# Kernel optimization log

Measured on AMD Instinct MI355X. Metric: run time of the kernel, lower is better.

Reference implementation:

```python
import jax, jax.numpy as jnp
import numpy as np

B, NPTS, NBOX = 16, 100000, 64
PTS_THRESHOLD = 2048          # topk voxels kept per scene
GT_THRESHOLD = 2.5            # distance multiplier
VOXEL_SIZE = 0.01
TENSOR_STRIDE = 8             # stride of the level being pruned
SIZE = TENSOR_STRIDE * VOXEL_SIZE  # 0.08, per-voxel cell size at this level


def setup_inputs() -> dict:
    key = jax.random.key(0)
    k1, k2, k3 = jax.random.split(key, 3)
    scores = jax.random.normal(k1, (B, NPTS), dtype=jnp.float32)
    points = jax.random.uniform(k2, (B, NPTS, 3), dtype=jnp.float32)
    gt_centers = jax.random.uniform(k3, (B, NBOX, 3), dtype=jnp.float32)
    return {"scores": scores, "points": points, "gt_centers": gt_centers}


def reference(scores, points, gt_centers):
    # --- per-batch topk score mask (MEFPN3D._get_score_mask) ---
    _, idx = jax.lax.top_k(scores, PTS_THRESHOLD)          # [B, K]
    score_mask = jnp.zeros(scores.shape, dtype=bool)
    score_mask = score_mask.at[jnp.arange(B)[:, None], idx].set(True)  # scatter True

    # --- gt distance mask (MEFPN3D._get_gt_mask) ---
    # distances: [B, Npts, n_boxes]
    diff = points[:, :, None, :] - gt_centers[:, None, :, :]
    distances = jnp.sqrt(jnp.sum(diff * diff, axis=-1))
    gt_mask = jnp.any(distances < SIZE * GT_THRESHOLD, axis=-1)        # [B, Npts]

    # --- combined prune mask (scatter of per-batch masks into global mask) ---
    prune_mask = jnp.logical_or(score_mask, gt_mask)

    # --- per-voxel sigmoid BCE loss, reduction='none' (CrossEntropyLoss use_sigmoid=True) ---
    target = gt_mask.astype(scores.dtype)
    losses = target * jax.nn.softplus(-scores) + (1.0 - target) * jax.nn.softplus(scores)
    return prune_mask, losses
```

## Files before the change

kernel.cpp:

```cpp
#include <hip/hip_runtime.h>
#include <hip/hip_bf16.h>
#include <stdint.h>

#define BB 16
#define NPTS 100000
#define NBOX 64
#define KTOP 2048
#define THRF 0.2f
#define C_LO 0.039984f
#define C_HI 0.040016f

#define SLICES 16
#define SLICE_SPAN 6272
#define SCAP 512
#define LIST_CAP 4096
#define CUT 0xC0000000u

#define CAND_OFF 0
#define CNT_OFF  (BB * SLICES * SCAP)
#define STATE_OFF (CNT_OFF + BB * SLICES)
#define TBOX_OFF  (STATE_OFF + BB * 2)

__device__ __forceinline__ uint32_t fmap(float f) {
    uint32_t b = __float_as_uint(f);
    return (b & 0x80000000u) ? ~b : (b | 0x80000000u);
}

__global__ __launch_bounds__(256) void cand_k(const float* __restrict__ scores,
                                              uint32_t* __restrict__ ws) {
    __shared__ uint32_t buf[SCAP];
    __shared__ uint32_t lcnt;
    const int b = blockIdx.y, sl = blockIdx.x, tid = threadIdx.x;
    if (tid == 0) lcnt = 0;
    __syncthreads();
    const int start = sl * SLICE_SPAN;
    const int nf4 = min(SLICE_SPAN, NPTS - start) >> 2;
    const float4* sc4 = reinterpret_cast<const float4*>(scores + (size_t)b * NPTS + start);
    for (int i4 = tid; i4 < nf4; i4 += 256) {
        const float4 v = sc4[i4];
        const uint32_t u[4] = {fmap(v.x), fmap(v.y), fmap(v.z), fmap(v.w)};
#pragma unroll
        for (int j = 0; j < 4; ++j) {
            if (u[j] >= CUT) {
                const uint32_t pos = atomicAdd(&lcnt, 1u);
                if (pos < SCAP) buf[pos] = u[j];
            }
        }
    }
    __syncthreads();
    const uint32_t c = lcnt;
    uint32_t* dst = ws + CAND_OFF + ((size_t)(b * SLICES + sl)) * SCAP;
    const uint32_t cw = c < SCAP ? c : SCAP;
    for (uint32_t i = tid; i < cw; i += 256) dst[i] = buf[i];
    if (tid == 0) ws[CNT_OFF + b * SLICES + sl] = c;
}

__device__ __forceinline__ void pick256(const uint32_t* __restrict__ hist,
                                        uint32_t* __restrict__ excl,
                                        int tid, int lane, uint32_t target,
                                        uint32_t* sBin, uint32_t* sKrem,
                                        uint32_t* sE, uint32_t* sTot, int wantE) {
    __syncthreads();
    if (tid < 64) {
        const uint32_t v0 = hist[4*tid], v1 = hist[4*tid+1], v2 = hist[4*tid+2], v3 = hist[4*tid+3];
        const uint32_t lt = v0 + v1 + v2 + v3;
        uint32_t x = lt;
#pragma unroll
        for (int off = 1; off < 64; off <<= 1) {
            const uint32_t y = __shfl_up(x, off);
            if (lane >= off) x += y;
        }
        const uint32_t ex = x - lt;
        excl[4*tid] = ex; excl[4*tid+1] = ex + v0;
        excl[4*tid+2] = ex + v0 + v1; excl[4*tid+3] = ex + v0 + v1 + v2;
        if (tid == 63) *sTot = x;
    }
    __syncthreads();
    {
        const uint32_t total = *sTot, lim = total - target;
        const uint32_t pe = excl[tid];
        const uint32_t pe1 = (tid == 255) ? total : excl[tid + 1];
        if (pe <= lim && pe1 > lim) {
            *sBin = (uint32_t)tid;
            *sKrem = target - (total - pe1);
            if (wantE) *sE = pe1 - pe;
        }
    }
    __syncthreads();
}

__global__ __launch_bounds__(256) void selfin_k(const float* __restrict__ scores,
                                                const float* __restrict__ ctrs,
                                                uint32_t* __restrict__ ws) {
    const int b = blockIdx.x, tid = threadIdx.x, w = tid >> 6, lane = tid & 63;
    __shared__ uint32_t list[LIST_CAP];
    __shared__ uint32_t h4[4][257];
    __shared__ uint32_t hist[256], excl[256];
    __shared__ uint32_t scnt[SLICES], soff[SLICES];
    __shared__ uint32_t wcnt[4];
    __shared__ uint32_t sBin, sKrem, sE, sTot, sIstar, sRun, sSpec, sUni, lcnt;

    const float* sc = scores + (size_t)b * NPTS;

    if (tid < NBOX) {
        const float cx = ctrs[(size_t)b * NBOX * 3 + 3 * tid];
        const float cy = ctrs[(size_t)b * NBOX * 3 + 3 * tid + 1];
        const float cz = ctrs[(size_t)b * NBOX * 3 + 3 * tid + 2];
        float4* TB = reinterpret_cast<float4*>(ws + TBOX_OFF) + b * NBOX;
        TB[tid] = make_float4(-2.0f * cx, -2.0f * cy, -2.0f * cz,
                              fmaf(cx, cx, fmaf(cy, cy, cz * cz)));
    }

    if (tid < SLICES) scnt[tid] = ws[CNT_OFF + b * SLICES + tid];
    __syncthreads();
    if (tid == 0) {
        uint32_t tot = 0; bool ok = true;
        for (int s = 0; s < SLICES; ++s) {
            soff[s] = tot;
            const uint32_t c = scnt[s];
            if (c > SCAP) ok = false;
            tot += c;
        }
        sTot = tot;
        sSpec = (ok && tot >= KTOP && tot <= LIST_CAP) ? 1u : 0u;
        sKrem = KTOP;
        sIstar = NPTS;
        lcnt = 0;
        sUni = 1u;
    }
    __syncthreads();

    uint32_t cnt, prefix = 0u;
    int shift0;
    if (sSpec) {
        cnt = sTot;
#pragma unroll 2
        for (int s = 0; s < SLICES; ++s) {
            const uint32_t c = scnt[s], o = soff[s];
            const uint32_t* src = ws + CAND_OFF + ((size_t)(b * SLICES + s)) * SCAP;
            for (uint32_t i = tid; i < c; i += 256) list[o + i] = src[i];
        }
        __syncthreads();
        const uint32_t b0 = list[0] >> 24;
        bool uni = true;
        for (uint32_t i = tid; i < cnt; i += 256) uni &= ((list[i] >> 24) == b0);
        if (!uni) atomicAnd(&sUni, 0u);
        __syncthreads();
        if (sUni) { prefix = b0 << 24; shift0 = 16; }
        else      { prefix = 0u;       shift0 = 24; }
    } else {
        for (int i = tid; i < 4 * 257; i += 256) (&h4[0][0])[i] = 0;
        __syncthreads();
        const float4* sc4 = reinterpret_cast<const float4*>(sc);
        for (int i4 = tid; i4 < NPTS / 4; i4 += 256) {
            const float4 v = sc4[i4];
            atomicAdd(&h4[w][fmap(v.x) >> 24], 1u);
            atomicAdd(&h4[w][fmap(v.y) >> 24], 1u);
            atomicAdd(&h4[w][fmap(v.z) >> 24], 1u);
            atomicAdd(&h4[w][fmap(v.w) >> 24], 1u);
        }
        __syncthreads();
        hist[tid] = h4[0][tid] + h4[1][tid] + h4[2][tid] + h4[3][tid];
        pick256(hist, excl, tid, lane, KTOP, &sBin, &sKrem, &sE, &sTot, 0);
        const uint32_t beta = sBin;
        for (int i4 = tid; i4 < NPTS / 4; i4 += 256) {
            const float4 v = sc4[i4];
            const uint32_t u[4] = {fmap(v.x), fmap(v.y), fmap(v.z), fmap(v.w)};
#pragma unroll
            for (int j = 0; j < 4; ++j) {
                if ((u[j] >> 24) == beta) {
                    const uint32_t pos = atomicAdd(&lcnt, 1u);
                    if (pos < LIST_CAP) list[pos] = u[j];
                }
            }
        }
        __syncthreads();
        cnt = lcnt < LIST_CAP ? lcnt : LIST_CAP;
        prefix = beta << 24;
        shift0 = 16;
    }

#pragma unroll 1
    for (int shift = shift0; shift >= 0; shift -= 8) {
        for (int i = tid; i < 4 * 257; i += 256) (&h4[0][0])[i] = 0;
        __syncthreads();
        const uint32_t hi8 = (shift < 24) ? (prefix >> (shift + 8)) : 0u;
        uint32_t* mh = h4[lane & 3];
        for (uint32_t i = tid; i < cnt; i += 256) {
            const uint32_t uu = list[i];
            const bool m = (shift == 24) || ((uu >> (shift + 8)) == hi8);
            if (m) atomicAdd(&mh[(uu >> shift) & 255u], 1u);
        }
        __syncthreads();
        hist[tid] = h4[0][tid] + h4[1][tid] + h4[2][tid] + h4[3][tid];
        const uint32_t target = sKrem;
        pick256(hist, excl, tid, lane, target, &sBin, &sKrem, &sE, &sTot,
                shift == 0 ? 1 : 0);
        prefix |= sBin << shift;
    }

    const uint32_t R = sKrem, E = sE;
    const uint32_t tbits = (prefix & 0x80000000u) ? (prefix & 0x7fffffffu) : ~prefix;

    if (E != R) {
        const float T = __uint_as_float(tbits);
        if (tid == 0) sRun = 0;
        __syncthreads();
        for (int base = 0; base < NPTS; base += 256) {
            const uint32_t r0 = sRun;
            if (r0 > R) break;
            const int i = base + tid;
            const bool eq = (i < NPTS) && (sc[i] == T);
            const unsigned long long mask = __ballot(eq);
            if (lane == 0) wcnt[w] = (uint32_t)__popcll(mask);
            __syncthreads();
            uint32_t before = 0, total = 0;
#pragma unroll
            for (int ww = 0; ww < 4; ++ww) {
                const uint32_t c = wcnt[ww];
                if (ww < w) before += c;
                total += c;
            }
            if (eq) {
                const uint32_t rank = r0 + before +
                    (uint32_t)__popcll(mask & ((1ull << lane) - 1ull));
                if (rank == R) sIstar = (uint32_t)i;
            }
            __syncthreads();
            if (tid == 0) sRun = r0 + total;
            __syncthreads();
        }
        __syncthreads();
    }
    if (tid == 0) {
        uint32_t* st = ws + STATE_OFF + b * 2;
        st[0] = tbits;
        st[1] = sIstar;
    }
}

__device__ __noinline__ bool exact_gt(float px, float py, float pz,
                                      const float* __restrict__ C) {
    bool hit = false;
#pragma unroll 1
    for (int k = 0; k < NBOX; ++k) {
        float dx = px - C[3 * k + 0];
        float dy = py - C[3 * k + 1];
        float dz = pz - C[3 * k + 2];
        float d2 = __fadd_rn(__fadd_rn(__fmul_rn(dx, dx), __fmul_rn(dy, dy)),
                             __fmul_rn(dz, dz));
        if (__fsqrt_rn(d2) < THRF) hit = true;
    }
    return hit;
}

__global__ __launch_bounds__(256) void main_k(const float* __restrict__ scores,
                                              const float* __restrict__ points,
                                              const float* __restrict__ ctrs,
                                              const uint32_t* __restrict__ ws,
                                              float* __restrict__ out) {
    const int b = blockIdx.y;
    const int i = blockIdx.x * 256 + threadIdx.x;
    if (i >= NPTS) return;

    const uint32_t* st = ws + STATE_OFF + b * 2;
    const float T = __uint_as_float(st[0]);
    const uint32_t Istar = st[1];
    const float4* __restrict__ TB =
        reinterpret_cast<const float4*>(ws + TBOX_OFF) + b * NBOX;

    const float* P = points + ((size_t)b * NPTS + i) * 3;
    const float px = P[0], py = P[1], pz = P[2];
    float m2 = 1e30f;

#pragma unroll
    for (int k = 0; k < NBOX; ++k) {
        const float4 B = TB[k];
        const float t = fmaf(B.x, px, fmaf(B.y, py, fmaf(B.z, pz, B.w)));
        m2 = fminf(m2, t);
    }

    const float s = scores[(size_t)b * NPTS + i];
    const float pp = fmaf(px, px, fmaf(py, py, pz * pz));
    const float m = pp + m2;
    bool gt;
    if (m < C_LO) gt = true;
    else if (m >= C_HI) gt = false;
    else gt = exact_gt(px, py, pz, ctrs + b * NBOX * 3);
    const bool sm = (s > T) || (s == T && (uint32_t)i < Istar);
    const float x = gt ? -s : s;
    const float ls = fmaxf(x, 0.0f) + __logf(1.0f + __expf(-fabsf(s)));
    out[(size_t)b * NPTS + i] = (gt || sm) ? 1.0f : 0.0f;
    out[(size_t)BB * NPTS + (size_t)b * NPTS + i] = ls;
}

extern "C" void kernel_launch(void* const* d_in, const int* in_sizes, int n_in,
                              void* d_out, int out_size, void* d_ws, size_t ws_size,
                              hipStream_t stream) {
    const float* scores = (const float*)d_in[0];
    const float* points = (const float*)d_in[1];
    const float* ctrs   = (const float*)d_in[2];
    float* out = (float*)d_out;
    uint32_t* ws = (uint32_t*)d_ws;

    const dim3 gridC(SLICES, BB);
    cand_k<<<gridC, 256, 0, stream>>>(scores, ws);
    selfin_k<<<BB, 256, 0, stream>>>(scores, ctrs, ws);
    const dim3 gridP((NPTS + 255) / 256, BB);
    main_k<<<gridP, 256, 0, stream>>>(scores, points, ctrs, ws, out);
}
```

Before: 47.70 us.

## Process eight points per thread in main kernel with vectorized loads and stores

The main kernel now has each thread handle eight consecutive points. It loads their coordinates and scores as float4 vectors and writes both outputs as float4 stores. Box centers are read directly from the input and shared across the eight points, so the precomputed box table in the selection kernel is dropped. This is meant to cut per-point load overhead, reuse box constants across points and widen memory transactions, at the cost of more registers and fewer threads.

```diff
diff --git a/kernel.cpp b/kernel.cpp
--- a/kernel.cpp
+++ b/kernel.cpp
@@ -19,7 +19,6 @@
 #define CAND_OFF 0
 #define CNT_OFF  (BB * SLICES * SCAP)
 #define STATE_OFF (CNT_OFF + BB * SLICES)
-#define TBOX_OFF  (STATE_OFF + BB * 2)
 
 __device__ __forceinline__ uint32_t fmap(float f) {
     uint32_t b = __float_as_uint(f);
@@ -99,18 +98,7 @@
     __shared__ uint32_t scnt[SLICES], soff[SLICES];
     __shared__ uint32_t wcnt[4];
     __shared__ uint32_t sBin, sKrem, sE, sTot, sIstar, sRun, sSpec, sUni, lcnt;
-
     const float* sc = scores + (size_t)b * NPTS;
-
-    if (tid < NBOX) {
-        const float cx = ctrs[(size_t)b * NBOX * 3 + 3 * tid];
-        const float cy = ctrs[(size_t)b * NBOX * 3 + 3 * tid + 1];
-        const float cz = ctrs[(size_t)b * NBOX * 3 + 3 * tid + 2];
-        float4* TB = reinterpret_cast<float4*>(ws + TBOX_OFF) + b * NBOX;
-        TB[tid] = make_float4(-2.0f * cx, -2.0f * cy, -2.0f * cz,
-                              fmaf(cx, cx, fmaf(cy, cy, cz * cz)));
-    }
-
     if (tid < SLICES) scnt[tid] = ws[CNT_OFF + b * SLICES + tid];
     __syncthreads();
     if (tid == 0) {
@@ -123,13 +111,9 @@
         }
         sTot = tot;
         sSpec = (ok && tot >= KTOP && tot <= LIST_CAP) ? 1u : 0u;
-        sKrem = KTOP;
-        sIstar = NPTS;
-        lcnt = 0;
-        sUni = 1u;
-    }
-    __syncthreads();
-
+        sKrem = KTOP; sIstar = NPTS; lcnt = 0; sUni = 1u;
+    }
+    __syncthreads();
     uint32_t cnt, prefix = 0u;
     int shift0;
     if (sSpec) {
@@ -176,10 +160,8 @@
         }
         __syncthreads();
         cnt = lcnt < LIST_CAP ? lcnt : LIST_CAP;
-        prefix = beta << 24;
-        shift0 = 16;
-    }
-
+        prefix = beta << 24; shift0 = 16;
+    }
 #pragma unroll 1
     for (int shift = shift0; shift >= 0; shift -= 8) {
         for (int i = tid; i < 4 * 257; i += 256) (&h4[0][0])[i] = 0;
@@ -194,14 +176,11 @@
         __syncthreads();
         hist[tid] = h4[0][tid] + h4[1][tid] + h4[2][tid] + h4[3][tid];
         const uint32_t target = sKrem;
-        pick256(hist, excl, tid, lane, target, &sBin, &sKrem, &sE, &sTot,
-                shift == 0 ? 1 : 0);
+        pick256(hist, excl, tid, lane, target, &sBin, &sKrem, &sE, &sTot, shift == 0 ? 1 : 0);
         prefix |= sBin << shift;
     }
-
     const uint32_t R = sKrem, E = sE;
     const uint32_t tbits = (prefix & 0x80000000u) ? (prefix & 0x7fffffffu) : ~prefix;
-
     if (E != R) {
         const float T = __uint_as_float(tbits);
         if (tid == 0) sRun = 0;
@@ -222,8 +201,7 @@
                 total += c;
             }
             if (eq) {
-                const uint32_t rank = r0 + before +
-                    (uint32_t)__popcll(mask & ((1ull << lane) - 1ull));
+                const uint32_t rank = r0 + before + (uint32_t)__popcll(mask & ((1ull << lane) - 1ull));
                 if (rank == R) sIstar = (uint32_t)i;
             }
             __syncthreads();
@@ -233,9 +211,8 @@
         __syncthreads();
     }
     if (tid == 0) {
-        uint32_t* st = ws + STATE_OFF + b * 2;
-        st[0] = tbits;
-        st[1] = sIstar;
+        ws[STATE_OFF + b * 2] = tbits;
+        ws[STATE_OFF + b * 2 + 1] = sIstar;
     }
 }
 
@@ -254,44 +231,67 @@
     return hit;
 }
 
+#define PPT 8
 __global__ __launch_bounds__(256) void main_k(const float* __restrict__ scores,
                                               const float* __restrict__ points,
                                               const float* __restrict__ ctrs,
                                               const uint32_t* __restrict__ ws,
                                               float* __restrict__ out) {
     const int b = blockIdx.y;
-    const int i = blockIdx.x * 256 + threadIdx.x;
-    if (i >= NPTS) return;
-
-    const uint32_t* st = ws + STATE_OFF + b * 2;
-    const float T = __uint_as_float(st[0]);
-    const uint32_t Istar = st[1];
-    const float4* __restrict__ TB =
-        reinterpret_cast<const float4*>(ws + TBOX_OFF) + b * NBOX;
-
-    const float* P = points + ((size_t)b * NPTS + i) * 3;
-    const float px = P[0], py = P[1], pz = P[2];
-    float m2 = 1e30f;
-
-#pragma unroll
+    const int i0 = (blockIdx.x * 256 + threadIdx.x) * PPT;
+    if (i0 >= NPTS) return;
+
+    const float T = __uint_as_float(ws[STATE_OFF + b * 2]);
+    const uint32_t Istar = ws[STATE_OFF + b * 2 + 1];
+    const float* __restrict__ C = ctrs + (size_t)b * NBOX * 3;
+
+    const float4* P4 = reinterpret_cast<const float4*>(points + ((size_t)b * NPTS + i0) * 3);
+    float4 q[6];
+#pragma unroll
+    for (int j = 0; j < 6; ++j) q[j] = P4[j];
+    const float* pf = reinterpret_cast<const float*>(q);
+    float qx[PPT], qy[PPT], qz[PPT], pp[PPT], m2[PPT];
+#pragma unroll
+    for (int j = 0; j < PPT; ++j) {
+        const float px = pf[3*j], py = pf[3*j+1], pz = pf[3*j+2];
+        qx[j] = -2.0f * px; qy[j] = -2.0f * py; qz[j] = -2.0f * pz;
+        pp[j] = fmaf(px, px, fmaf(py, py, pz * pz));
+        m2[j] = 1e30f;
+    }
+
+#pragma unroll 4
     for (int k = 0; k < NBOX; ++k) {
-        const float4 B = TB[k];
-        const float t = fmaf(B.x, px, fmaf(B.y, py, fmaf(B.z, pz, B.w)));
-        m2 = fminf(m2, t);
-    }
-
-    const float s = scores[(size_t)b * NPTS + i];
-    const float pp = fmaf(px, px, fmaf(py, py, pz * pz));
-    const float m = pp + m2;
-    bool gt;
-    if (m < C_LO) gt = true;
-    else if (m >= C_HI) gt = false;
-    else gt = exact_gt(px, py, pz, ctrs + b * NBOX * 3);
-    const bool sm = (s > T) || (s == T && (uint32_t)i < Istar);
-    const float x = gt ? -s : s;
-    const float ls = fmaxf(x, 0.0f) + __logf(1.0f + __expf(-fabsf(s)));
-    out[(size_t)b * NPTS + i] = (gt || sm) ? 1.0f : 0.0f;
-    out[(size_t)BB * NPTS + (size_t)b * NPTS + i] = ls;
+        const float cx = C[3*k], cy = C[3*k+1], cz = C[3*k+2];
+        const float cc = fmaf(cx, cx, fmaf(cy, cy, cz * cz));
+#pragma unroll
+        for (int j = 0; j < PPT; ++j) {
+            const float t = fmaf(cx, qx[j], fmaf(cy, qy[j], fmaf(cz, qz[j], cc)));
+            m2[j] = fminf(m2[j], t);
+        }
+    }
+
+    const float4* S4 = reinterpret_cast<const float4*>(scores + (size_t)b * NPTS + i0);
+    float4 sv[2] = {S4[0], S4[1]};
+    const float* s = reinterpret_cast<const float*>(sv);
+    float pr[PPT], ls[PPT];
+#pragma unroll
+    for (int j = 0; j < PPT; ++j) {
+        const float m = pp[j] + m2[j];
+        bool gt;
+        if (m < C_LO) gt = true;
+        else if (m >= C_HI) gt = false;
+        else gt = exact_gt(pf[3*j], pf[3*j+1], pf[3*j+2], C);
+        const bool sm = (s[j] > T) || (s[j] == T && (uint32_t)(i0 + j) < Istar);
+        pr[j] = (gt || sm) ? 1.0f : 0.0f;
+        const float x = gt ? -s[j] : s[j];
+        ls[j] = fmaxf(x, 0.0f) + __logf(1.0f + __expf(-fabsf(s[j])));
+    }
+    float4* o0 = reinterpret_cast<float4*>(out + (size_t)b * NPTS + i0);
+    float4* o1 = reinterpret_cast<float4*>(out + (size_t)BB * NPTS + (size_t)b * NPTS + i0);
+    o0[0] = make_float4(pr[0], pr[1], pr[2], pr[3]);
+    o0[1] = make_float4(pr[4], pr[5], pr[6], pr[7]);
+    o1[0] = make_float4(ls[0], ls[1], ls[2], ls[3]);
+    o1[1] = make_float4(ls[4], ls[5], ls[6], ls[7]);
 }
 
 extern "C" void kernel_launch(void* const* d_in, const int* in_sizes, int n_in,
@@ -306,6 +306,6 @@
     const dim3 gridC(SLICES, BB);
     cand_k<<<gridC, 256, 0, stream>>>(scores, ws);
     selfin_k<<<BB, 256, 0, stream>>>(scores, ctrs, ws);
-    const dim3 gridP((NPTS + 255) / 256, BB);
+    const dim3 gridP((NPTS / PPT + 255) / 256, BB);
     main_k<<<gridP, 256, 0, stream>>>(scores, points, ctrs, ws, out);
 }
```

New measurement: 55.79 us. +16.9%, slower.
